# Optimization experiments

Measured on AMD Instinct MI355X. Metric: run time of the kernel, lower is better.

Reference implementation:

```python
import jax, jax.numpy as jnp
import numpy as np

B, L, V, D, H = 4096, 32, 50000, 300, 6
HD = D // H  # 50


def setup_inputs() -> dict:
    key = jax.random.key(0)
    ks = jax.random.split(key, 9)
    s = 0.02
    return {
        "title": jax.random.randint(ks[0], (B, L), 0, V),
        "emb": jax.random.normal(ks[1], (V, D), dtype=jnp.float32) * s,
        "pos_emb": jax.random.normal(ks[2], (512, D), dtype=jnp.float32) * s,
        "Wq": jax.random.normal(ks[3], (D, D), dtype=jnp.float32) * s,
        "bq": jnp.zeros((D,), jnp.float32),
        "Wk": jax.random.normal(ks[4], (D, D), dtype=jnp.float32) * s,
        "bk": jnp.zeros((D,), jnp.float32),
        "Wv": jax.random.normal(ks[5], (D, D), dtype=jnp.float32) * s,
        "bv": jnp.zeros((D,), jnp.float32),
        "Wo": jax.random.normal(ks[6], (D, D), dtype=jnp.float32) * s,
        "bo": jnp.zeros((D,), jnp.float32),
        "Va": jax.random.normal(ks[7], (D, D), dtype=jnp.float32) * s,
        "ba": jnp.zeros((D,), jnp.float32),
        "qw": jax.random.normal(ks[8], (D, 1), dtype=jnp.float32) * s,
    }


def reference(title, emb, pos_emb, Wq, bq, Wk, bk, Wv, bv, Wo, bo, Va, ba, qw):
    b, l = title.shape
    # word embedding + positional embedding
    x = emb[title] + pos_emb[:l][None, :, :]  # [B, L, D]

    def heads(y):  # [B, L, D] -> [B, H, L, HD]
        return y.reshape(b, l, H, HD).transpose(0, 2, 1, 3)

    # manual multi-head self-attention (mask is all-ones -> no masking effect)
    q = heads(x @ Wq.T + bq) / jnp.sqrt(jnp.float32(HD))
    k = heads(x @ Wk.T + bk)
    v = heads(x @ Wv.T + bv)
    scores = jnp.einsum("bhqd,bhkd->bhqk", q, k)  # [B, H, L, L]
    w = jax.nn.softmax(scores, axis=-1)  # dropout is identity in eval
    ctx = jnp.einsum("bhqk,bhkd->bhqd", w, v)
    ctx = ctx.transpose(0, 2, 1, 3).reshape(b, l, D)
    ctx = ctx @ Wo.T + bo  # [B, L, D]

    # additive attention pooling
    t = jnp.tanh(ctx @ Va.T + ba)          # [B, L, D]
    a = (t @ qw)[..., 0]                    # [B, L]
    alpha = jax.nn.softmax(a, axis=1)       # [B, L]
    out = jnp.einsum("bs,bsd->bd", alpha, ctx)  # [B, D]
    return out
```

## Files before the change

### kernel.cpp

```cpp
#include <hip/hip_runtime.h>
#include <math.h>

typedef _Float16 f16;
typedef _Float16 half8 __attribute__((ext_vector_type(8)));
typedef _Float16 half4 __attribute__((ext_vector_type(4)));
typedef float float4v __attribute__((ext_vector_type(4)));
typedef int int4v __attribute__((ext_vector_type(4)));

#define MFMA16(a, b, c) __builtin_amdgcn_mfma_f32_16x16x32_f16((a), (b), (c), 0, 0, 0)


#define WQKV_OFF 0u
#define BQKV_OFF 655360u
#define WO_OFF   659456u
#define WVA_OFF  864256u
#define BVA_OFF  1069056u
#define CBAR_OFF 1070336u

__device__ __forceinline__ float fast_tanh(float x) {
    float e = __expf(2.f * x);
    return 1.f - 2.f / (e + 1.f);
}

__global__ void repack1(const float* __restrict__ Wq, const float* __restrict__ Wk,
                        const float* __restrict__ Wv, const float* __restrict__ Wo,
                        const float* __restrict__ bq, const float* __restrict__ bk,
                        const float* __restrict__ bv,
                        f16* __restrict__ wqkvF, f16* __restrict__ wo16F,
                        float* __restrict__ bqkv) {
    int idx = blockIdx.x * 256 + threadIdx.x;
    const float rs = 0.14142135623730951f;
    if (idx < 327680) {
        int ntile = idx / 5120, rem = idx - ntile * 5120;
        int ks = rem / 512, r2 = rem - ks * 512;
        int lane = r2 >> 3, j = r2 & 7;
        int n = ntile * 16 + (lane & 15);
        int k = ks * 32 + (lane >> 4) * 8 + j;
        int g = n / 320, r = n - g * 320;
        float v = 0.f;
        if (r < 300 && k < 300) {
            if (g == 0) v = Wq[r * 300 + k] * rs;
            else if (g == 1) v = Wk[r * 300 + k];
            else if (g == 2) v = Wv[r * 300 + k];
        }
        wqkvF[idx] = (f16)v;
    } else if (idx < 430080) {
        int t = idx - 327680;
        int ntile = t / 5120, rem = t - ntile * 5120;
        int ks = rem / 512, r2 = rem - ks * 512;
        int lane = r2 >> 3, j = r2 & 7;
        int n = ntile * 16 + (lane & 15);
        int k = ks * 32 + (lane >> 4) * 8 + j;
        wo16F[t] = (f16)((n < 300 && k < 300) ? Wo[n * 300 + k] : 0.f);
    } else if (idx < 431104) {
        int n = idx - 430080;
        int g = n / 320, r = n - g * 320;
        float v = 0.f;
        if (r < 300) {
            if (g == 0) v = bq[r] * rs;
            else if (g == 1) v = bk[r];
            else if (g == 2) v = bv[r];
        }
        bqkv[n] = v;
    }
}

__global__ void repack2(const float* __restrict__ Va, const float* __restrict__ Wo,
                        f16* __restrict__ wvaF) {
    int bt = blockIdx.x;
    int mt = bt / 20, nt = bt % 20;
    int lane = threadIdx.x & 63;
    int lr = lane & 15, quad = lane >> 4;
    float4v acc = {0.f, 0.f, 0.f, 0.f};
    int m = mt * 16 + lr;
    int nn = nt * 16 + lr;
    for (int ks = 0; ks < 10; ++ks) {
        int c = ks * 32 + quad * 8;
        half8 af, bf;
#pragma unroll
        for (int j = 0; j < 8; ++j) {
            int cc = c + j;
            af[j] = (f16)((m < 300 && cc < 300) ? Va[m * 300 + cc] : 0.f);
            bf[j] = (f16)((nn < 300 && cc < 300) ? Wo[cc * 300 + nn] : 0.f);
        }
        acc = MFMA16(af, bf, acc);
    }
#pragma unroll
    for (int r = 0; r < 4; ++r) {
        int row = mt * 16 + quad * 4 + r;
        int col = nt * 16 + lr;
        int addr = ((row >> 4) * 10 + (col >> 5)) * 512 +
                   (((col >> 3) & 3) * 16 + (row & 15)) * 8 + (col & 7);
        wvaF[addr] = (f16)acc[r];
    }
}

__global__ void repack3(const float* __restrict__ Va, const float* __restrict__ bo,
                        const float* __restrict__ ba, float* __restrict__ bva) {
    int j = blockIdx.x;
    int lane = threadIdx.x;
    float s = 0.f;
    if (j < 300) {
        for (int k = lane; k < 300; k += 64) s += Va[j * 300 + k] * bo[k];
    }
#pragma unroll
    for (int off = 1; off < 64; off <<= 1) s += __shfl_xor(s, off, 64);
    if (lane == 0) bva[j] = (j < 300) ? s + ba[j] : 0.f;
}

__global__ __launch_bounds__(512, 4) void qkvattn_kernel(
    const int* __restrict__ title, const float* __restrict__ emb,
    const float* __restrict__ pos,
    const f16* __restrict__ wqkvF, const float* __restrict__ bqkv,
    const f16* __restrict__ wvaF, const float* __restrict__ bva,
    const float* __restrict__ qw, f16* __restrict__ cbar) {
    __shared__ __align__(16) f16 qL[6 * 32 * 72];
    __shared__ __align__(16) f16 kL[6 * 32 * 72];
    __shared__ __align__(16) f16 vT[6 * 64 * 32];
    __shared__ float aL[32];
    const int ib = blockIdx.x, tid = threadIdx.x;
    const int w = tid >> 6, lane = tid & 63, lr = lane & 15, quad = lane >> 4;
    const float4v vz = {0.f, 0.f, 0.f, 0.f};
    const int4v z4 = {0, 0, 0, 0};
    f16* xA = vT;

    for (int u = tid; u < 1280; u += 512) {
        int fragblk = u >> 6, lu = u & 63;
        int mt = fragblk / 10, ks = fragblk - mt * 10;
        int row = mt * 16 + (lu & 15);
        int col = ks * 32 + (lu >> 4) * 8;
        int t = title[ib * 32 + row];
        half8 h;
        if (col + 8 <= 300) {
            float4v e0 = *(const float4v*)&emb[t * 300 + col];
            float4v e1 = *(const float4v*)&emb[t * 300 + col + 4];
            float4v p0 = *(const float4v*)&pos[row * 300 + col];
            float4v p1 = *(const float4v*)&pos[row * 300 + col + 4];
#pragma unroll
            for (int j = 0; j < 4; ++j) {
                h[j] = (f16)(e0[j] + p0[j]);
                h[4 + j] = (f16)(e1[j] + p1[j]);
            }
        } else {
#pragma unroll
            for (int j = 0; j < 8; ++j) {
                int cc = col + j;
                h[j] = (f16)((cc < 300) ? emb[t * 300 + cc] + pos[row * 300 + cc] : 0.f);
            }
        }
        *(half8*)&xA[u * 8] = h;
    }
    for (int i = tid; i < 1344; i += 512) {
        int hrow = i / 7, c = i - hrow * 7;
        ((int*)&qL[hrow * 72 + 50])[c] = 0;
        ((int*)&kL[hrow * 72 + 50])[c] = 0;
    }
    if (tid < 32) aL[tid] = 0.f;
    float bb[8];
#pragma unroll
    for (int j = 0; j < 8; ++j) bb[j] = bqkv[(w * 8 + j) * 16 + lr];
    __syncthreads();

    float4v acc[2][8];
#pragma unroll
    for (int mt = 0; mt < 2; ++mt)
#pragma unroll
        for (int j = 0; j < 8; ++j) acc[mt][j] = vz;
#pragma unroll
    for (int ks = 0; ks < 10; ++ks) {
        half8 a0 = *(const half8*)&xA[(ks * 64 + lane) * 8];
        half8 a1 = *(const half8*)&xA[((10 + ks) * 64 + lane) * 8];
#pragma unroll
        for (int j = 0; j < 8; ++j) {
            int tile = w * 8 + j;
            if (tile < 60) {
                half8 bf = *(const half8*)&wqkvF[((tile * 10 + ks) * 64 + lane) * 8];
                acc[0][j] = MFMA16(a0, bf, acc[0][j]);
                acc[1][j] = MFMA16(a1, bf, acc[1][j]);
            }
        }
    }
    __syncthreads();

    for (int i = tid; i < 336; i += 512) {
        int t = i >> 2, c4 = i & 3;
        int h = t / 14, d = 50 + (t - (t / 14) * 14);
        ((int4v*)&vT[(h * 64 + d) * 32])[c4] = z4;
    }
#pragma unroll
    for (int j = 0; j < 8; ++j) {
        int tile = w * 8 + j;
        int wi = tile / 20;
        int n = tile * 16 + lr;
        int cc = n - wi * 320;
        if (wi < 3 && cc < 300) {
            int h = cc / 50, d = cc - h * 50;
            if (wi == 2) {
#pragma unroll
                for (int mt = 0; mt < 2; ++mt) {
                    int row0 = mt * 16 + quad * 4;
                    half4 pk;
#pragma unroll
                    for (int r = 0; r < 4; ++r) pk[r] = (f16)(acc[mt][j][r] + bb[j]);
                    int idx = (h * 64 + d) * 32 + row0;
                    int byt = (idx * 2) ^ (((d >> 2) & 3) << 4);
                    *(half4*)((char*)vT + byt) = pk;
                }
            } else {
                f16* dst = (wi == 0) ? qL : kL;
#pragma unroll
                for (int mt = 0; mt < 2; ++mt)
#pragma unroll
                    for (int r = 0; r < 4; ++r) {
                        int row = mt * 16 + quad * 4 + r;
                        dst[(h * 32 + row) * 72 + d] = (f16)(acc[mt][j][r] + bb[j]);
                    }
            }
        }
    }
    __syncthreads();

    const int hh = w;
    if (w < 6) {
        float4v s00 = vz, s01 = vz, s10 = vz, s11 = vz;
#pragma unroll
        for (int ks = 0; ks < 2; ++ks) {
            int c = ks * 32 + quad * 8;
            half8 aq0 = *(const half8*)&qL[(hh * 32 + lr) * 72 + c];
            half8 aq1 = *(const half8*)&qL[(hh * 32 + 16 + lr) * 72 + c];
            half8 bk0 = *(const half8*)&kL[(hh * 32 + lr) * 72 + c];
            half8 bk1 = *(const half8*)&kL[(hh * 32 + 16 + lr) * 72 + c];
            s00 = MFMA16(aq0, bk0, s00);
            s01 = MFMA16(aq0, bk1, s01);
            s10 = MFMA16(aq1, bk0, s10);
            s11 = MFMA16(aq1, bk1, s11);
        }
        f16* ph = qL + hh * 32 * 72;
#pragma unroll
        for (int mt = 0; mt < 2; ++mt) {
            float4v sv0 = mt ? s10 : s00;
            float4v sv1 = mt ? s11 : s01;
#pragma unroll
            for (int r = 0; r < 4; ++r) {
                float v0 = sv0[r], v1 = sv1[r];
                float m = fmaxf(v0, v1);
#pragma unroll
                for (int off = 1; off < 16; off <<= 1) m = fmaxf(m, __shfl_xor(m, off, 64));
                float e0 = __expf(v0 - m), e1 = __expf(v1 - m);
                float ss = e0 + e1;
#pragma unroll
                for (int off = 1; off < 16; off <<= 1) ss += __shfl_xor(ss, off, 64);
                float inv = 1.0f / ss;
                int row = mt * 16 + quad * 4 + r;
                ph[row * 40 + lr] = (f16)(e0 * inv);
                ph[row * 40 + 16 + lr] = (f16)(e1 * inv);
            }
        }
    }
    __syncthreads();

    f16* scratch = kL;
    for (int i = tid; i < 32 * 28; i += 512) {
        int row = i / 28, cc = 300 + (i - row * 28);
        scratch[row * 328 + cc] = (f16)0.f;
    }
    if (w < 6) {
        int h = hh;
        f16* ph = qL + hh * 32 * 72;
        half8 aw0 = *(const half8*)&ph[lr * 40 + quad * 8];
        half8 aw1 = *(const half8*)&ph[(16 + lr) * 40 + quad * 8];
        float4v c0[4], c1[4];
#pragma unroll
        for (int nt = 0; nt < 4; ++nt) { c0[nt] = vz; c1[nt] = vz; }
#pragma unroll
        for (int nt = 0; nt < 4; ++nt) {
            int rIdx = nt * 16 + lr;
            int idx = (hh * 64 + rIdx) * 32 + quad * 8;
            int byt = (idx * 2) ^ (((rIdx >> 2) & 3) << 4);
            half8 bvf = *(const half8*)((const char*)vT + byt);
            c0[nt] = MFMA16(aw0, bvf, c0[nt]);
            c1[nt] = MFMA16(aw1, bvf, c1[nt]);
        }
#pragma unroll
        for (int mt = 0; mt < 2; ++mt)
#pragma unroll
            for (int nt = 0; nt < 4; ++nt)
#pragma unroll
                for (int r = 0; r < 4; ++r) {
                    int d = nt * 16 + lr;
                    if (d < 50) {
                        int row = mt * 16 + quad * 4 + r;
                        float4v cv = mt ? c1[nt] : c0[nt];
                        scratch[row * 328 + h * 50 + d] = (f16)cv[r];
                    }
                }
    }

    const int mtile = w >> 2, nsub = w & 3;
    half8 pbf[5];
    float pbva[5], pqw[5];
#pragma unroll
    for (int i = 0; i < 5; ++i) {
        int n = (nsub * 5 + i) * 16 + lr;
        pbf[i] = *(const half8*)&wvaF[(((nsub * 5 + i) * 10) * 64 + lane) * 8];
        pbva[i] = bva[n];
        pqw[i] = (n < 300) ? qw[n] : 0.f;
    }
    __syncthreads();

    {
        float4v vacc[5];
#pragma unroll
        for (int i = 0; i < 5; ++i) vacc[i] = vz;
        const int arow = (mtile * 16 + lr) * 328;
        {
            half8 a = *(const half8*)&scratch[arow + quad * 8];
#pragma unroll
            for (int i = 0; i < 5; ++i) vacc[i] = MFMA16(a, pbf[i], vacc[i]);
        }
#pragma unroll
        for (int ks = 1; ks < 10; ++ks) {
            half8 a = *(const half8*)&scratch[arow + ks * 32 + quad * 8];
#pragma unroll
            for (int i = 0; i < 5; ++i) {
                half8 bf = *(const half8*)&wvaF[((((nsub * 5 + i) * 10) + ks) * 64 + lane) * 8];
                vacc[i] = MFMA16(a, bf, vacc[i]);
            }
        }
        float ps[4] = {0.f, 0.f, 0.f, 0.f};
#pragma unroll
        for (int i = 0; i < 5; ++i) {
#pragma unroll
            for (int r = 0; r < 4; ++r) ps[r] += fast_tanh(vacc[i][r] + pbva[i]) * pqw[i];
        }
#pragma unroll
        for (int r = 0; r < 4; ++r)
#pragma unroll
            for (int off = 1; off < 16; off <<= 1) ps[r] += __shfl_xor(ps[r], off, 64);
        if (lr == 0) {
#pragma unroll
            for (int r = 0; r < 4; ++r) atomicAdd(&aL[mtile * 16 + quad * 4 + r], ps[r]);
        }
    }
    __syncthreads();

    {
        float av = aL[lane & 31];
        float m5 = av;
#pragma unroll
        for (int off = 1; off < 32; off <<= 1) m5 = fmaxf(m5, __shfl_xor(m5, off, 32));
        float e5 = __expf(av - m5);
        float ss5 = e5;
#pragma unroll
        for (int off = 1; off < 32; off <<= 1) ss5 += __shfl_xor(ss5, off, 32);
        float al = e5 / ss5;
        if (tid < 320) {
            int d = tid;
            float acc6 = 0.f;
#pragma unroll
            for (int l = 0; l < 32; ++l)
                acc6 += __shfl(al, l, 32) * (float)scratch[l * 328 + d];
            cbar[ib * 320 + d] = (f16)acc6;
        }
    }
}

__global__ __launch_bounds__(512) void out_kernel(
    const f16* __restrict__ cbar, const f16* __restrict__ wo16F,
    const float* __restrict__ bo, float* __restrict__ out) {
    __shared__ __align__(16) f16 cA[32 * 328];
    const int mb = blockIdx.x, tid = threadIdx.x;
    const int w = tid >> 6, lane = tid & 63, lr = lane & 15, quad = lane >> 4;
    const int mh = w >> 2, nsub = w & 3;
    for (int i = tid; i < 1280; i += 512) {
        int row = i / 40, g = i - row * 40;
        *(half8*)&cA[row * 328 + g * 8] = *(const half8*)&cbar[(mb * 32 + row) * 320 + g * 8];
    }
    __syncthreads();
    const float4v vz = {0.f, 0.f, 0.f, 0.f};
    float4v acc[5];
#pragma unroll
    for (int i = 0; i < 5; ++i) acc[i] = vz;
#pragma unroll
    for (int ks = 0; ks < 10; ++ks) {
        half8 a = *(const half8*)&cA[(mh * 16 + lr) * 328 + ks * 32 + quad * 8];
#pragma unroll
        for (int i = 0; i < 5; ++i) {
            half8 bf = *(const half8*)&wo16F[((((nsub * 5 + i) * 10) + ks) * 64 + lane) * 8];
            acc[i] = MFMA16(a, bf, acc[i]);
        }
    }
#pragma unroll
    for (int i = 0; i < 5; ++i) {
        int n = (nsub * 5 + i) * 16 + lr;
        if (n < 300) {
            float bb = bo[n];
#pragma unroll
            for (int r = 0; r < 4; ++r)
                out[(mb * 32 + mh * 16 + quad * 4 + r) * 300 + n] = acc[i][r] + bb;
        }
    }
}

extern "C" void kernel_launch(void* const* d_in, const int* in_sizes, int n_in,
                              void* d_out, int out_size, void* d_ws, size_t ws_size,
                              hipStream_t stream) {
    const int* title = (const int*)d_in[0];
    const float* emb = (const float*)d_in[1];
    const float* pos = (const float*)d_in[2];
    const float* Wq = (const float*)d_in[3];
    const float* bq = (const float*)d_in[4];
    const float* Wk = (const float*)d_in[5];
    const float* bk = (const float*)d_in[6];
    const float* Wv = (const float*)d_in[7];
    const float* bv = (const float*)d_in[8];
    const float* Wo = (const float*)d_in[9];
    const float* bo = (const float*)d_in[10];
    const float* Va = (const float*)d_in[11];
    const float* ba = (const float*)d_in[12];
    const float* qw = (const float*)d_in[13];
    char* ws = (char*)d_ws;
    float* out = (float*)d_out;

    f16* wqkvF = (f16*)(ws + WQKV_OFF);
    float* bqkv = (float*)(ws + BQKV_OFF);
    f16* wo16F = (f16*)(ws + WO_OFF);
    f16* wvaF = (f16*)(ws + WVA_OFF);
    float* bva = (float*)(ws + BVA_OFF);
    f16* cbar = (f16*)(ws + CBAR_OFF);

    repack1<<<1684, 256, 0, stream>>>(Wq, Wk, Wv, Wo, bq, bk, bv, wqkvF, wo16F, bqkv);
    repack2<<<400, 64, 0, stream>>>(Va, Wo, wvaF);
    repack3<<<320, 64, 0, stream>>>(Va, bo, ba, bva);
    qkvattn_kernel<<<4096, 512, 0, stream>>>(title, emb, pos, wqkvF, bqkv, wvaF, bva, qw, cbar);
    out_kernel<<<128, 512, 0, stream>>>(cbar, wo16F, bo, out);
}
```

Baseline: 431.2 us.

## Merge repack kernels and fuse output projection into attention kernel

Combines the three weight-repack kernels into one launch, with blocks dispatched by range. Moves the final Wo projection into the main attention kernel through a shared-memory cbar vector, which removes the cbar global round trip and the separate out_kernel launch. Title indices are now loaded up front, before the embedding gather, so their latency can overlap. The trade-off is that each block runs a single-row MFMA that uses only 1/16 of the output tile, repeated over 4096 blocks, which wastes matrix throughput and adds Wo reads from L2.

```diff
diff --git a/kernel.cpp b/kernel.cpp
--- a/kernel.cpp
+++ b/kernel.cpp
@@ -15,97 +15,95 @@
 #define WO_OFF   659456u
 #define WVA_OFF  864256u
 #define BVA_OFF  1069056u
-#define CBAR_OFF 1070336u
 
 __device__ __forceinline__ float fast_tanh(float x) {
     float e = __expf(2.f * x);
     return 1.f - 2.f / (e + 1.f);
 }
 
-__global__ void repack1(const float* __restrict__ Wq, const float* __restrict__ Wk,
-                        const float* __restrict__ Wv, const float* __restrict__ Wo,
-                        const float* __restrict__ bq, const float* __restrict__ bk,
-                        const float* __restrict__ bv,
-                        f16* __restrict__ wqkvF, f16* __restrict__ wo16F,
-                        float* __restrict__ bqkv) {
-    int idx = blockIdx.x * 256 + threadIdx.x;
+__global__ __launch_bounds__(256) void repack_all(
+    const float* __restrict__ Wq, const float* __restrict__ Wk,
+    const float* __restrict__ Wv, const float* __restrict__ Wo,
+    const float* __restrict__ bq, const float* __restrict__ bk,
+    const float* __restrict__ bv, const float* __restrict__ Va,
+    const float* __restrict__ bo, const float* __restrict__ ba,
+    f16* __restrict__ wqkvF, f16* __restrict__ wo16F, float* __restrict__ bqkv,
+    f16* __restrict__ wvaF, float* __restrict__ bva) {
+    const int bid = blockIdx.x, tid = threadIdx.x;
     const float rs = 0.14142135623730951f;
-    if (idx < 327680) {
-        int ntile = idx / 5120, rem = idx - ntile * 5120;
-        int ks = rem / 512, r2 = rem - ks * 512;
-        int lane = r2 >> 3, j = r2 & 7;
-        int n = ntile * 16 + (lane & 15);
-        int k = ks * 32 + (lane >> 4) * 8 + j;
-        int g = n / 320, r = n - g * 320;
-        float v = 0.f;
-        if (r < 300 && k < 300) {
-            if (g == 0) v = Wq[r * 300 + k] * rs;
-            else if (g == 1) v = Wk[r * 300 + k];
-            else if (g == 2) v = Wv[r * 300 + k];
-        }
-        wqkvF[idx] = (f16)v;
-    } else if (idx < 430080) {
-        int t = idx - 327680;
-        int ntile = t / 5120, rem = t - ntile * 5120;
-        int ks = rem / 512, r2 = rem - ks * 512;
-        int lane = r2 >> 3, j = r2 & 7;
-        int n = ntile * 16 + (lane & 15);
-        int k = ks * 32 + (lane >> 4) * 8 + j;
-        wo16F[t] = (f16)((n < 300 && k < 300) ? Wo[n * 300 + k] : 0.f);
-    } else if (idx < 431104) {
-        int n = idx - 430080;
-        int g = n / 320, r = n - g * 320;
-        float v = 0.f;
-        if (r < 300) {
-            if (g == 0) v = bq[r] * rs;
-            else if (g == 1) v = bk[r];
-            else if (g == 2) v = bv[r];
-        }
-        bqkv[n] = v;
-    }
-}
-
-__global__ void repack2(const float* __restrict__ Va, const float* __restrict__ Wo,
-                        f16* __restrict__ wvaF) {
-    int bt = blockIdx.x;
-    int mt = bt / 20, nt = bt % 20;
-    int lane = threadIdx.x & 63;
-    int lr = lane & 15, quad = lane >> 4;
-    float4v acc = {0.f, 0.f, 0.f, 0.f};
-    int m = mt * 16 + lr;
-    int nn = nt * 16 + lr;
-    for (int ks = 0; ks < 10; ++ks) {
-        int c = ks * 32 + quad * 8;
-        half8 af, bf;
-#pragma unroll
-        for (int j = 0; j < 8; ++j) {
-            int cc = c + j;
-            af[j] = (f16)((m < 300 && cc < 300) ? Va[m * 300 + cc] : 0.f);
-            bf[j] = (f16)((nn < 300 && cc < 300) ? Wo[cc * 300 + nn] : 0.f);
-        }
-        acc = MFMA16(af, bf, acc);
-    }
-#pragma unroll
-    for (int r = 0; r < 4; ++r) {
-        int row = mt * 16 + quad * 4 + r;
-        int col = nt * 16 + lr;
-        int addr = ((row >> 4) * 10 + (col >> 5)) * 512 +
-                   (((col >> 3) & 3) * 16 + (row & 15)) * 8 + (col & 7);
-        wvaF[addr] = (f16)acc[r];
-    }
-}
-
-__global__ void repack3(const float* __restrict__ Va, const float* __restrict__ bo,
-                        const float* __restrict__ ba, float* __restrict__ bva) {
-    int j = blockIdx.x;
-    int lane = threadIdx.x;
-    float s = 0.f;
-    if (j < 300) {
-        for (int k = lane; k < 300; k += 64) s += Va[j * 300 + k] * bo[k];
-    }
-#pragma unroll
-    for (int off = 1; off < 64; off <<= 1) s += __shfl_xor(s, off, 64);
-    if (lane == 0) bva[j] = (j < 300) ? s + ba[j] : 0.f;
+    if (bid < 1684) {
+        int idx = bid * 256 + tid;
+        if (idx < 327680) {
+            int ntile = idx / 5120, rem = idx - ntile * 5120;
+            int ks = rem / 512, r2 = rem - ks * 512;
+            int lane = r2 >> 3, j = r2 & 7;
+            int n = ntile * 16 + (lane & 15);
+            int k = ks * 32 + (lane >> 4) * 8 + j;
+            int g = n / 320, r = n - g * 320;
+            float v = 0.f;
+            if (r < 300 && k < 300) {
+                if (g == 0) v = Wq[r * 300 + k] * rs;
+                else if (g == 1) v = Wk[r * 300 + k];
+                else if (g == 2) v = Wv[r * 300 + k];
+            }
+            wqkvF[idx] = (f16)v;
+        } else if (idx < 430080) {
+            int t = idx - 327680;
+            int ntile = t / 5120, rem = t - ntile * 5120;
+            int ks = rem / 512, r2 = rem - ks * 512;
+            int lane = r2 >> 3, j = r2 & 7;
+            int n = ntile * 16 + (lane & 15);
+            int k = ks * 32 + (lane >> 4) * 8 + j;
+            wo16F[t] = (f16)((n < 300 && k < 300) ? Wo[n * 300 + k] : 0.f);
+        } else if (idx < 431104) {
+            int n = idx - 430080;
+            int g = n / 320, r = n - g * 320;
+            float v = 0.f;
+            if (r < 300) {
+                if (g == 0) v = bq[r] * rs;
+                else if (g == 1) v = bk[r];
+                else if (g == 2) v = bv[r];
+            }
+            bqkv[n] = v;
+        }
+    } else if (bid < 1784) {
+        int bt = (bid - 1684) * 4 + (tid >> 6);
+        int mt = bt / 20, nt = bt % 20;
+        int lane = tid & 63;
+        int lr = lane & 15, quad = lane >> 4;
+        float4v acc = {0.f, 0.f, 0.f, 0.f};
+        int m = mt * 16 + lr;
+        int nn = nt * 16 + lr;
+        for (int ks = 0; ks < 10; ++ks) {
+            int c = ks * 32 + quad * 8;
+            half8 af, bf;
+#pragma unroll
+            for (int j = 0; j < 8; ++j) {
+                int cc = c + j;
+                af[j] = (f16)((m < 300 && cc < 300) ? Va[m * 300 + cc] : 0.f);
+                bf[j] = (f16)((nn < 300 && cc < 300) ? Wo[cc * 300 + nn] : 0.f);
+            }
+            acc = MFMA16(af, bf, acc);
+        }
+#pragma unroll
+        for (int r = 0; r < 4; ++r) {
+            int row = mt * 16 + quad * 4 + r;
+            int col = nt * 16 + lr;
+            int addr = ((row >> 4) * 10 + (col >> 5)) * 512 +
+                       (((col >> 3) & 3) * 16 + (row & 15)) * 8 + (col & 7);
+            wvaF[addr] = (f16)acc[r];
+        }
+    } else {
+        int j = (bid - 1784) * 4 + (tid >> 6);
+        int lane = tid & 63;
+        float s = 0.f;
+        if (j < 300) {
+            for (int k = lane; k < 300; k += 64) s += Va[j * 300 + k] * bo[k];
+        }
+#pragma unroll
+        for (int off = 1; off < 64; off <<= 1) s += __shfl_xor(s, off, 64);
+        if (lane == 0) bva[j] = (j < 300) ? s + ba[j] : 0.f;
+    }
 }
 
 __global__ __launch_bounds__(512, 4) void qkvattn_kernel(
@@ -113,10 +111,12 @@
     const float* __restrict__ pos,
     const f16* __restrict__ wqkvF, const float* __restrict__ bqkv,
     const f16* __restrict__ wvaF, const float* __restrict__ bva,
-    const float* __restrict__ qw, f16* __restrict__ cbar) {
+    const float* __restrict__ qw, const f16* __restrict__ wo16F,
+    const float* __restrict__ bo, float* __restrict__ out) {
     __shared__ __align__(16) f16 qL[6 * 32 * 72];
     __shared__ __align__(16) f16 kL[6 * 32 * 72];
     __shared__ __align__(16) f16 vT[6 * 64 * 32];
+    __shared__ __align__(16) f16 cbarL[320];
     __shared__ float aL[32];
     const int ib = blockIdx.x, tid = threadIdx.x;
     const int w = tid >> 6, lane = tid & 63, lr = lane & 15, quad = lane >> 4;
@@ -124,31 +124,45 @@
     const int4v z4 = {0, 0, 0, 0};
     f16* xA = vT;
 
-    for (int u = tid; u < 1280; u += 512) {
-        int fragblk = u >> 6, lu = u & 63;
-        int mt = fragblk / 10, ks = fragblk - mt * 10;
-        int row = mt * 16 + (lu & 15);
-        int col = ks * 32 + (lu >> 4) * 8;
-        int t = title[ib * 32 + row];
-        half8 h;
-        if (col + 8 <= 300) {
-            float4v e0 = *(const float4v*)&emb[t * 300 + col];
-            float4v e1 = *(const float4v*)&emb[t * 300 + col + 4];
-            float4v p0 = *(const float4v*)&pos[row * 300 + col];
-            float4v p1 = *(const float4v*)&pos[row * 300 + col + 4];
-#pragma unroll
-            for (int j = 0; j < 4; ++j) {
-                h[j] = (f16)(e0[j] + p0[j]);
-                h[4 + j] = (f16)(e1[j] + p1[j]);
-            }
-        } else {
-#pragma unroll
-            for (int j = 0; j < 8; ++j) {
-                int cc = col + j;
-                h[j] = (f16)((cc < 300) ? emb[t * 300 + cc] + pos[row * 300 + cc] : 0.f);
-            }
-        }
-        *(half8*)&xA[u * 8] = h;
+    int tt[3];
+#pragma unroll
+    for (int ii = 0; ii < 3; ++ii) {
+        int u = tid + ii * 512;
+        if (u < 1280) {
+            int lu = u & 63;
+            int row = ((u >> 6) / 10) * 16 + (lu & 15);
+            tt[ii] = title[ib * 32 + row];
+        }
+    }
+#pragma unroll
+    for (int ii = 0; ii < 3; ++ii) {
+        int u = tid + ii * 512;
+        if (u < 1280) {
+            int fragblk = u >> 6, lu = u & 63;
+            int mt = fragblk / 10, ks = fragblk - mt * 10;
+            int row = mt * 16 + (lu & 15);
+            int col = ks * 32 + (lu >> 4) * 8;
+            int t = tt[ii];
+            half8 h;
+            if (col + 8 <= 300) {
+                float4v e0 = *(const float4v*)&emb[t * 300 + col];
+                float4v e1 = *(const float4v*)&emb[t * 300 + col + 4];
+                float4v p0 = *(const float4v*)&pos[row * 300 + col];
+                float4v p1 = *(const float4v*)&pos[row * 300 + col + 4];
+#pragma unroll
+                for (int j = 0; j < 4; ++j) {
+                    h[j] = (f16)(e0[j] + p0[j]);
+                    h[4 + j] = (f16)(e1[j] + p1[j]);
+                }
+            } else {
+#pragma unroll
+                for (int j = 0; j < 8; ++j) {
+                    int cc = col + j;
+                    h[j] = (f16)((cc < 300) ? emb[t * 300 + cc] + pos[row * 300 + cc] : 0.f);
+                }
+            }
+            *(half8*)&xA[u * 8] = h;
+        }
     }
     for (int i = tid; i < 1344; i += 512) {
         int hrow = i / 7, c = i - hrow * 7;
@@ -360,44 +374,25 @@
 #pragma unroll
             for (int l = 0; l < 32; ++l)
                 acc6 += __shfl(al, l, 32) * (float)scratch[l * 328 + d];
-            cbar[ib * 320 + d] = (f16)acc6;
-        }
-    }
-}
-
-__global__ __launch_bounds__(512) void out_kernel(
-    const f16* __restrict__ cbar, const f16* __restrict__ wo16F,
-    const float* __restrict__ bo, float* __restrict__ out) {
-    __shared__ __align__(16) f16 cA[32 * 328];
-    const int mb = blockIdx.x, tid = threadIdx.x;
-    const int w = tid >> 6, lane = tid & 63, lr = lane & 15, quad = lane >> 4;
-    const int mh = w >> 2, nsub = w & 3;
-    for (int i = tid; i < 1280; i += 512) {
-        int row = i / 40, g = i - row * 40;
-        *(half8*)&cA[row * 328 + g * 8] = *(const half8*)&cbar[(mb * 32 + row) * 320 + g * 8];
-    }
-    __syncthreads();
-    const float4v vz = {0.f, 0.f, 0.f, 0.f};
-    float4v acc[5];
-#pragma unroll
-    for (int i = 0; i < 5; ++i) acc[i] = vz;
-#pragma unroll
-    for (int ks = 0; ks < 10; ++ks) {
-        half8 a = *(const half8*)&cA[(mh * 16 + lr) * 328 + ks * 32 + quad * 8];
-#pragma unroll
-        for (int i = 0; i < 5; ++i) {
-            half8 bf = *(const half8*)&wo16F[((((nsub * 5 + i) * 10) + ks) * 64 + lane) * 8];
-            acc[i] = MFMA16(a, bf, acc[i]);
-        }
-    }
-#pragma unroll
-    for (int i = 0; i < 5; ++i) {
-        int n = (nsub * 5 + i) * 16 + lr;
-        if (n < 300) {
-            float bb = bo[n];
-#pragma unroll
-            for (int r = 0; r < 4; ++r)
-                out[(mb * 32 + mh * 16 + quad * 4 + r) * 300 + n] = acc[i][r] + bb;
+            cbarL[d] = (f16)acc6;
+        }
+    }
+    __syncthreads();
+
+    {
+        half8 af[10];
+#pragma unroll
+        for (int ks = 0; ks < 10; ++ks)
+            af[ks] = *(const half8*)&cbarL[ks * 32 + quad * 8];
+        for (int t = w; t < 19; t += 8) {
+            float4v oacc = vz;
+#pragma unroll
+            for (int ks = 0; ks < 10; ++ks) {
+                half8 bf = *(const half8*)&wo16F[((t * 10 + ks) * 64 + lane) * 8];
+                oacc = MFMA16(af[ks], bf, oacc);
+            }
+            int n = t * 16 + lr;
+            if (quad == 0 && n < 300) out[ib * 300 + n] = oacc[0] + bo[n];
         }
     }
 }
@@ -427,11 +422,9 @@
     f16* wo16F = (f16*)(ws + WO_OFF);
     f16* wvaF = (f16*)(ws + WVA_OFF);
     float* bva = (float*)(ws + BVA_OFF);
-    f16* cbar = (f16*)(ws + CBAR_OFF);
-
-    repack1<<<1684, 256, 0, stream>>>(Wq, Wk, Wv, Wo, bq, bk, bv, wqkvF, wo16F, bqkv);
-    repack2<<<400, 64, 0, stream>>>(Va, Wo, wvaF);
-    repack3<<<320, 64, 0, stream>>>(Va, bo, ba, bva);
-    qkvattn_kernel<<<4096, 512, 0, stream>>>(title, emb, pos, wqkvF, bqkv, wvaF, bva, qw, cbar);
-    out_kernel<<<128, 512, 0, stream>>>(cbar, wo16F, bo, out);
+
+    repack_all<<<1864, 256, 0, stream>>>(Wq, Wk, Wv, Wo, bq, bk, bv, Va, bo, ba,
+                                         wqkvF, wo16F, bqkv, wvaF, bva);
+    qkvattn_kernel<<<4096, 512, 0, stream>>>(title, emb, pos, wqkvF, bqkv, wvaF, bva,
+                                             qw, wo16F, bo, out);
 }
```

Measured after the change: 449.6 us. 1.04x slower.
